# Optimization experiments

Measured on AMD Instinct MI355X. Metric: run time of the kernel, lower is better.

The kernel has to match this reference:

```python
import jax, jax.numpy as jnp
import numpy as np

BN_EPS = 1e-5
N_NODES = 100000
N_EDGES = 300000
IN_FEAT = 256
HIDDEN = 128
N_ETYPES = 4


def setup_inputs() -> dict:
    key = jax.random.key(0)
    ks = jax.random.split(key, 10)
    s = 1.0 / np.sqrt(2 * IN_FEAT)
    return {
        "h_src": jax.random.normal(ks[0], (N_NODES, IN_FEAT), jnp.float32),
        "h_dst": jax.random.normal(ks[1], (N_NODES, IN_FEAT), jnp.float32),
        "src_nodes": jax.random.randint(ks[2], (N_EDGES,), 0, N_NODES),
        "dst_nodes": jax.random.randint(ks[3], (N_EDGES,), 0, N_NODES),
        "etype_idx": 0,
        "W1": jax.random.normal(ks[4], (2 * IN_FEAT, HIDDEN), jnp.float32) * s,
        "b1": jnp.zeros((HIDDEN,), jnp.float32),
        "bn_gamma": jnp.ones((HIDDEN,), jnp.float32),
        "bn_beta": jnp.zeros((HIDDEN,), jnp.float32),
        "bn_mean": jnp.zeros((HIDDEN,), jnp.float32),
        "bn_var": jnp.ones((HIDDEN,), jnp.float32),
        "emb": jax.random.normal(ks[5], (N_ETYPES, HIDDEN), jnp.float32),
        "W2": jax.random.normal(ks[6], (HIDDEN, HIDDEN // 2), jnp.float32) * (1.0 / np.sqrt(HIDDEN)),
        "b2": jnp.zeros((HIDDEN // 2,), jnp.float32),
        "W3": jax.random.normal(ks[7], (HIDDEN // 2, 1), jnp.float32) * (1.0 / np.sqrt(HIDDEN // 2)),
        "b3": jnp.zeros((1,), jnp.float32),
    }


def reference(h_src, h_dst, src_nodes, dst_nodes, etype_idx,
              W1, b1, bn_gamma, bn_beta, bn_mean, bn_var,
              emb, W2, b2, W3, b3):
    # gather endpoint features and concat -> [E, 2*in_feat]
    src_feat = h_src[src_nodes]
    dst_feat = h_dst[dst_nodes]
    edge_feat = jnp.concatenate([src_feat, dst_feat], axis=1)
    # Linear + ReLU (Dropout is identity in eval) + BatchNorm1d (running stats)
    x = jax.nn.relu(edge_feat @ W1 + b1)
    x = (x - bn_mean) * jax.lax.rsqrt(bn_var + BN_EPS) * bn_gamma + bn_beta
    # add edge-type embedding (broadcast over edges)
    x = x + emb[etype_idx]
    # per-edge-type predictor MLP -> scalar score per edge
    x = jax.nn.relu(x @ W2 + b2)
    scores = (x @ W3 + b3).squeeze(-1)
    return scores
```

## Files before the change

kernel.cpp:

```cpp
#include <hip/hip_runtime.h>
#include <hip/hip_bf16.h>


typedef __attribute__((ext_vector_type(8))) short bf16x8;
typedef __attribute__((ext_vector_type(4))) float f32x4;

constexpr int HID   = 128;
constexpr int ETILE = 64;
constexpr int AS    = 136;

__device__ inline ushort f2bf(float f) {
    union { __hip_bfloat16 h; ushort u; } cv;
    cv.h = __float2bfloat16(f);
    return cv.u;
}

__global__ __launch_bounds__(256)
void prep_kernel(const float* __restrict__ W1, const float* __restrict__ W2,
                 const float* __restrict__ bn_gamma, const float* __restrict__ bn_beta,
                 const float* __restrict__ bn_mean, const float* __restrict__ bn_var,
                 const float* __restrict__ emb, const int* __restrict__ etype,
                 ushort* __restrict__ B1p, ushort* __restrict__ B2p,
                 float* __restrict__ sc, float* __restrict__ sh)
{
    int i = blockIdx.x * blockDim.x + threadIdx.x;
    if (i < 65536) {
        int j = i & 7, lane = (i >> 3) & 63, ct = (i >> 9) & 7, ks = i >> 12;
        int k = ks * 32 + (lane >> 4) * 8 + j;
        int c = ct * 16 + (lane & 15);
        B1p[i] = f2bf(W1[k * HID + c]);
    } else if (i < 65536 + 8192) {
        int p = i - 65536;
        int j = p & 7, lane = (p >> 3) & 63, ct = (p >> 9) & 3, ks = p >> 11;
        int k = ks * 32 + (lane >> 4) * 8 + j;
        int c = ct * 16 + (lane & 15);
        B2p[p] = f2bf(W2[k * 64 + c]);
    } else if (i < 65536 + 8192 + HID) {
        int c = i - 65536 - 8192;
        float s = bn_gamma[c] * rsqrtf(bn_var[c] + 1e-5f);
        sc[c] = s;
        sh[c] = bn_beta[c] - bn_mean[c] * s + emb[etype[0] * HID + c];
    }
}

__global__ __launch_bounds__(256)
void edge_mlp_mfma(const float* __restrict__ h_src, const float* __restrict__ h_dst,
                   const int* __restrict__ src_nodes, const int* __restrict__ dst_nodes,
                   const ushort* __restrict__ B1p, const ushort* __restrict__ B2p,
                   const float* __restrict__ b1, const float* __restrict__ sc,
                   const float* __restrict__ sh, const float* __restrict__ b2,
                   const float* __restrict__ W3, const float* __restrict__ b3,
                   float* __restrict__ out, int n_edges)
{
    __shared__ ushort sA[ETILE * AS];
    __shared__ int s_src[ETILE], s_dst[ETILE];

    const int t    = threadIdx.x;
    const int lane = t & 63;
    const int w    = t >> 6;
    const int lr   = lane & 15;
    const int lq   = lane >> 4;
    const int ebase = blockIdx.x * ETILE;

    if (t < ETILE) {
        int e = ebase + t;
        s_src[t] = src_nodes[e < n_edges ? e : 0];
    } else if (t < 2 * ETILE) {
        int e = ebase + t - ETILE;
        s_dst[t - ETILE] = dst_nodes[e < n_edges ? e : 0];
    }

    f32x4 acc[4][2];
#pragma unroll
    for (int rt = 0; rt < 4; ++rt)
#pragma unroll
        for (int c = 0; c < 2; ++c) acc[rt][c] = (f32x4)0.0f;

    for (int kc = 0; kc < 4; ++kc) {
        const float* hp   = (kc < 2) ? h_src : h_dst;
        const int*   sidx = (kc < 2) ? s_src : s_dst;
        const int    koff = (kc & 1) * 128;

        __syncthreads();

#pragma unroll
        for (int i = 0; i < 8; ++i) {
            int f = t + i * 256;
            int e = f >> 5, q = f & 31;
            const float4 v = *reinterpret_cast<const float4*>(
                hp + (size_t)sidx[e] * 256 + koff + q * 4);
            ushort4 b;
            b.x = f2bf(v.x); b.y = f2bf(v.y); b.z = f2bf(v.z); b.w = f2bf(v.w);
            *reinterpret_cast<ushort4*>(&sA[e * AS + q * 4]) = b;
        }
        __syncthreads();

#pragma unroll
        for (int ks = 0; ks < 4; ++ks) {
            const int kstep = kc * 4 + ks;
            bf16x8 bf0 = *reinterpret_cast<const bf16x8*>(
                B1p + (size_t)(((kstep * 8) + 2 * w) * 64 + lane) * 8);
            bf16x8 bf1 = *reinterpret_cast<const bf16x8*>(
                B1p + (size_t)(((kstep * 8) + 2 * w + 1) * 64 + lane) * 8);
#pragma unroll
            for (int rt = 0; rt < 4; ++rt) {
                bf16x8 af = *reinterpret_cast<const bf16x8*>(
                    &sA[(rt * 16 + lr) * AS + ks * 32 + lq * 8]);
                acc[rt][0] = __builtin_amdgcn_mfma_f32_16x16x32_bf16(af, bf0, acc[rt][0], 0, 0, 0);
                acc[rt][1] = __builtin_amdgcn_mfma_f32_16x16x32_bf16(af, bf1, acc[rt][1], 0, 0, 0);
            }
        }
    }

    __syncthreads();
#pragma unroll
    for (int ctl = 0; ctl < 2; ++ctl) {
        int c = (2 * w + ctl) * 16 + lr;
        float bb = b1[c], s = sc[c], z = sh[c];
#pragma unroll
        for (int rt = 0; rt < 4; ++rt)
#pragma unroll
            for (int r = 0; r < 4; ++r) {
                float x = fmaxf(acc[rt][ctl][r] + bb, 0.0f);
                sA[(rt * 16 + lq * 4 + r) * AS + c] = f2bf(fmaf(x, s, z));
            }
    }
    __syncthreads();

    f32x4 acc2[4];
#pragma unroll
    for (int ct = 0; ct < 4; ++ct) acc2[ct] = (f32x4)0.0f;

#pragma unroll
    for (int ks = 0; ks < 4; ++ks) {
        bf16x8 af = *reinterpret_cast<const bf16x8*>(
            &sA[(w * 16 + lr) * AS + ks * 32 + lq * 8]);
#pragma unroll
        for (int ct = 0; ct < 4; ++ct) {
            bf16x8 bf = *reinterpret_cast<const bf16x8*>(
                B2p + (size_t)((ks * 4 + ct) * 64 + lane) * 8);
            acc2[ct] = __builtin_amdgcn_mfma_f32_16x16x32_bf16(af, bf, acc2[ct], 0, 0, 0);
        }
    }

    float w3v[4], b2v[4];
#pragma unroll
    for (int ct = 0; ct < 4; ++ct) {
        int c = ct * 16 + lr;
        w3v[ct] = W3[c];
        b2v[ct] = b2[c];
    }
#pragma unroll
    for (int r = 0; r < 4; ++r) {
        float sum = 0.0f;
#pragma unroll
        for (int ct = 0; ct < 4; ++ct)
            sum += fmaxf(acc2[ct][r] + b2v[ct], 0.0f) * w3v[ct];
        sum += __shfl_xor(sum, 1);
        sum += __shfl_xor(sum, 2);
        sum += __shfl_xor(sum, 4);
        sum += __shfl_xor(sum, 8);
        int e = ebase + w * 16 + lq * 4 + r;
        if (lr == 0 && e < n_edges) out[e] = sum + b3[0];
    }
}

extern "C" void kernel_launch(void* const* d_in, const int* in_sizes, int n_in,
                              void* d_out, int out_size, void* d_ws, size_t ws_size,
                              hipStream_t stream) {
    const float* h_src     = (const float*)d_in[0];
    const float* h_dst     = (const float*)d_in[1];
    const int*   src_nodes = (const int*)d_in[2];
    const int*   dst_nodes = (const int*)d_in[3];
    const int*   etype     = (const int*)d_in[4];
    const float* W1        = (const float*)d_in[5];
    const float* b1        = (const float*)d_in[6];
    const float* bn_gamma  = (const float*)d_in[7];
    const float* bn_beta   = (const float*)d_in[8];
    const float* bn_mean   = (const float*)d_in[9];
    const float* bn_var    = (const float*)d_in[10];
    const float* emb       = (const float*)d_in[11];
    const float* W2        = (const float*)d_in[12];
    const float* b2        = (const float*)d_in[13];
    const float* W3        = (const float*)d_in[14];
    const float* b3        = (const float*)d_in[15];

    ushort* B1p = (ushort*)d_ws;
    ushort* B2p = B1p + 65536;
    float*  scp = (float*)(B2p + 8192);
    float*  shp = scp + HID;

    prep_kernel<<<(65536 + 8192 + HID + 255) / 256, 256, 0, stream>>>(
        W1, W2, bn_gamma, bn_beta, bn_mean, bn_var, emb, etype, B1p, B2p, scp, shp);

    const int n_edges = in_sizes[2];
    const int grid = (n_edges + ETILE - 1) / ETILE;
    edge_mlp_mfma<<<grid, 256, 0, stream>>>(h_src, h_dst, src_nodes, dst_nodes,
                                            B1p, B2p, b1, scp, shp, b2, W3, b3,
                                            (float*)d_out, n_edges);
}
```

Measured before the change: 103.6 us.

## Double-buffer gathered feature chunks in LDS with register prefetch

Splits the 512-wide K dimension into eight 64-wide chunks and keeps two LDS buffers. The global gather for the next chunk is issued into registers before the MFMA work on the current chunk, so gather latency can overlap with compute. The launch bounds now request 4 blocks per SM, and the second-layer activations reuse the combined buffer with the old stride. This adds register pressure from the prefetch registers and doubles the number of barriers, in exchange for hiding gather latency.

```diff
diff --git a/kernel.cpp b/kernel.cpp
--- a/kernel.cpp
+++ b/kernel.cpp
@@ -7,7 +7,8 @@
 
 constexpr int HID   = 128;
 constexpr int ETILE = 64;
-constexpr int AS    = 136;
+constexpr int AS    = 72;
+constexpr int XS    = 136;
 
 __device__ inline ushort f2bf(float f) {
     union { __hip_bfloat16 h; ushort u; } cv;
@@ -43,7 +44,7 @@
     }
 }
 
-__global__ __launch_bounds__(256)
+__global__ __launch_bounds__(256, 4)
 void edge_mlp_mfma(const float* __restrict__ h_src, const float* __restrict__ h_dst,
                    const int* __restrict__ src_nodes, const int* __restrict__ dst_nodes,
                    const ushort* __restrict__ B1p, const ushort* __restrict__ B2p,
@@ -52,7 +53,7 @@
                    const float* __restrict__ W3, const float* __restrict__ b3,
                    float* __restrict__ out, int n_edges)
 {
-    __shared__ ushort sA[ETILE * AS];
+    __shared__ ushort sA[2][ETILE * AS];
     __shared__ int s_src[ETILE], s_dst[ETILE];
 
     const int t    = threadIdx.x;
@@ -76,43 +77,66 @@
 #pragma unroll
         for (int c = 0; c < 2; ++c) acc[rt][c] = (f32x4)0.0f;
 
-    for (int kc = 0; kc < 4; ++kc) {
-        const float* hp   = (kc < 2) ? h_src : h_dst;
-        const int*   sidx = (kc < 2) ? s_src : s_dst;
-        const int    koff = (kc & 1) * 128;
-
-        __syncthreads();
-
-#pragma unroll
-        for (int i = 0; i < 8; ++i) {
-            int f = t + i * 256;
-            int e = f >> 5, q = f & 31;
-            const float4 v = *reinterpret_cast<const float4*>(
-                hp + (size_t)sidx[e] * 256 + koff + q * 4);
-            ushort4 b;
-            b.x = f2bf(v.x); b.y = f2bf(v.y); b.z = f2bf(v.z); b.w = f2bf(v.w);
-            *reinterpret_cast<ushort4*>(&sA[e * AS + q * 4]) = b;
-        }
-        __syncthreads();
-
-#pragma unroll
-        for (int ks = 0; ks < 4; ++ks) {
-            const int kstep = kc * 4 + ks;
-            bf16x8 bf0 = *reinterpret_cast<const bf16x8*>(
-                B1p + (size_t)(((kstep * 8) + 2 * w) * 64 + lane) * 8);
-            bf16x8 bf1 = *reinterpret_cast<const bf16x8*>(
-                B1p + (size_t)(((kstep * 8) + 2 * w + 1) * 64 + lane) * 8);
-#pragma unroll
-            for (int rt = 0; rt < 4; ++rt) {
-                bf16x8 af = *reinterpret_cast<const bf16x8*>(
-                    &sA[(rt * 16 + lr) * AS + ks * 32 + lq * 8]);
-                acc[rt][0] = __builtin_amdgcn_mfma_f32_16x16x32_bf16(af, bf0, acc[rt][0], 0, 0, 0);
-                acc[rt][1] = __builtin_amdgcn_mfma_f32_16x16x32_bf16(af, bf1, acc[rt][1], 0, 0, 0);
-            }
-        }
-    }
-
-    __syncthreads();
+    float4 rA[4], rB[4];
+
+#define LOADC(kc, R) do {                                                      \
+        const float* hp = ((kc) < 4) ? h_src : h_dst;                          \
+        const int* sidx = ((kc) < 4) ? s_src : s_dst;                          \
+        const int koff = ((kc) & 3) * 64;                                      \
+        _Pragma("unroll")                                                      \
+        for (int i = 0; i < 4; ++i) {                                          \
+            int f = t + i * 256; int e = f >> 4; int q = f & 15;               \
+            R[i] = *reinterpret_cast<const float4*>(                           \
+                hp + (size_t)sidx[e] * 256 + koff + q * 4);                    \
+        } } while (0)
+
+#define STOREC(B, R) do {                                                      \
+        _Pragma("unroll")                                                      \
+        for (int i = 0; i < 4; ++i) {                                          \
+            int f = t + i * 256; int e = f >> 4; int q = f & 15;               \
+            ushort4 bv;                                                        \
+            bv.x = f2bf(R[i].x); bv.y = f2bf(R[i].y);                          \
+            bv.z = f2bf(R[i].z); bv.w = f2bf(R[i].w);                          \
+            *reinterpret_cast<ushort4*>(&sA[B][e * AS + q * 4]) = bv;          \
+        } } while (0)
+
+#define COMP(kc, B) do {                                                       \
+        _Pragma("unroll")                                                      \
+        for (int ks = 0; ks < 2; ++ks) {                                       \
+            const int kstep = (kc) * 2 + ks;                                   \
+            bf16x8 bf0 = *reinterpret_cast<const bf16x8*>(                     \
+                B1p + (size_t)(((kstep * 8) + 2 * w) * 64 + lane) * 8);        \
+            bf16x8 bf1 = *reinterpret_cast<const bf16x8*>(                     \
+                B1p + (size_t)(((kstep * 8) + 2 * w + 1) * 64 + lane) * 8);    \
+            _Pragma("unroll")                                                  \
+            for (int rt = 0; rt < 4; ++rt) {                                   \
+                bf16x8 af = *reinterpret_cast<const bf16x8*>(                  \
+                    &sA[B][(rt * 16 + lr) * AS + ks * 32 + lq * 8]);           \
+                acc[rt][0] = __builtin_amdgcn_mfma_f32_16x16x32_bf16(af, bf0, acc[rt][0], 0, 0, 0); \
+                acc[rt][1] = __builtin_amdgcn_mfma_f32_16x16x32_bf16(af, bf1, acc[rt][1], 0, 0, 0); \
+            } } } while (0)
+
+    __syncthreads();
+    LOADC(0, rA);
+    STOREC(0, rA);
+    LOADC(1, rB);
+    __syncthreads();
+
+    LOADC(2, rA);  COMP(0, 0);  STOREC(1, rB);  __syncthreads();
+    LOADC(3, rB);  COMP(1, 1);  STOREC(0, rA);  __syncthreads();
+    LOADC(4, rA);  COMP(2, 0);  STOREC(1, rB);  __syncthreads();
+    LOADC(5, rB);  COMP(3, 1);  STOREC(0, rA);  __syncthreads();
+    LOADC(6, rA);  COMP(4, 0);  STOREC(1, rB);  __syncthreads();
+    LOADC(7, rB);  COMP(5, 1);  STOREC(0, rA);  __syncthreads();
+                   COMP(6, 0);  STOREC(1, rB);  __syncthreads();
+                   COMP(7, 1);
+
+#undef LOADC
+#undef STOREC
+#undef COMP
+
+    __syncthreads();
+    ushort* sX = &sA[0][0];
 #pragma unroll
     for (int ctl = 0; ctl < 2; ++ctl) {
         int c = (2 * w + ctl) * 16 + lr;
@@ -122,7 +146,7 @@
 #pragma unroll
             for (int r = 0; r < 4; ++r) {
                 float x = fmaxf(acc[rt][ctl][r] + bb, 0.0f);
-                sA[(rt * 16 + lq * 4 + r) * AS + c] = f2bf(fmaf(x, s, z));
+                sX[(rt * 16 + lq * 4 + r) * XS + c] = f2bf(fmaf(x, s, z));
             }
     }
     __syncthreads();
@@ -134,7 +158,7 @@
 #pragma unroll
     for (int ks = 0; ks < 4; ++ks) {
         bf16x8 af = *reinterpret_cast<const bf16x8*>(
-            &sA[(w * 16 + lr) * AS + ks * 32 + lq * 8]);
+            &sX[(w * 16 + lr) * XS + ks * 32 + lq * 8]);
 #pragma unroll
         for (int ct = 0; ct < 4; ++ct) {
             bf16x8 bf = *reinterpret_cast<const bf16x8*>(
```

Result: no change. 102.9 us (-0.7%).
